# Optimization experiments

Measured on AMD Instinct MI355X. Metric: run time of the kernel, lower is better.

Reference implementation:

```python
import jax, jax.numpy as jnp
import numpy as np
from jax.experimental import sparse as jsparse

N_ITEMS = 20000   # item catalog size (S is [N_ITEMS, N_ITEMS])
N_USERS = 2048    # user batch
NNZ = 4_000_000


def setup_inputs() -> dict:
    key = jax.random.key(0)
    k1, k2, k3, k4 = jax.random.split(key, 4)
    X = jax.random.normal(k1, (N_USERS, N_ITEMS), dtype=jnp.float32)
    S_vals = jax.random.normal(k2, (NNZ,), dtype=jnp.float32)
    S_rows = jax.random.randint(k3, (NNZ,), 0, N_ITEMS, dtype=jnp.int32)
    S_cols = jax.random.randint(k4, (NNZ,), 0, N_ITEMS, dtype=jnp.int32)
    return {"X": X, "S_vals": S_vals, "S_rows": S_rows, "S_cols": S_cols}


def reference(X, S_vals, S_rows, S_cols):
    # torch.sparse.mm(S, X.t()).t()  ==  X @ S^T, with S sparse COO.
    indices = jnp.stack([S_rows, S_cols], axis=1)  # [nnz, 2]
    S = jsparse.BCOO((S_vals, indices), shape=(N_ITEMS, N_ITEMS))
    # (S @ X^T)^T -> [n_users, n_items]; duplicate indices sum, matching COO semantics.
    return (S @ X.T).T
```

## Files before the change

### kernel.cpp

```cpp
#include <hip/hip_runtime.h>

#define N_ITEMS 20000
#define N_USERS 2048
#define NNZ     4000000
#define LDP     2112
#define HALF_ITEMS 10000
#define CAP     320

typedef float    f32x4 __attribute__((ext_vector_type(4)));
typedef int      i32x4 __attribute__((ext_vector_type(4)));
typedef unsigned u32x4 __attribute__((ext_vector_type(4)));

#define OFF_XT     ((size_t)0)
#define OFF_CSRPK  ((size_t)84480000)
#define OFF_CNT    (OFF_CSRPK + 25600000)

static __device__ __forceinline__ unsigned short f2bf(float f) {
  unsigned u = __float_as_uint(f);
  unsigned r = (u + 0x7fffu + ((u >> 16) & 1u)) >> 16;
  return (unsigned short)r;
}

#define NSQ ((NNZ / 4 + 255) / 256)
#define NT_BLOCKS (313 * 32)

static __device__ __forceinline__ void scatter_body(
    const int* __restrict__ rows, const int* __restrict__ cols,
    const float* __restrict__ vals, int* __restrict__ cnt,
    unsigned* __restrict__ csr_pk, int pass, int b) {
  int i = (b * 256 + (int)threadIdx.x) * 4;
  if (i < NNZ) {
    i32x4 r4 = __builtin_nontemporal_load(reinterpret_cast<const i32x4*>(rows + i));
    i32x4 c4 = __builtin_nontemporal_load(reinterpret_cast<const i32x4*>(cols + i));
    f32x4 v4 = __builtin_nontemporal_load(reinterpret_cast<const f32x4*>(vals + i));
    #pragma unroll
    for (int k = 0; k < 4; ++k) {
      int r = r4[k];
      if ((unsigned)(r - pass * HALF_ITEMS) < (unsigned)HALF_ITEMS) {
        int pos = atomicAdd(&cnt[r], 1);
        if (pos >= CAP) pos = CAP - 1;
        csr_pk[r * CAP + pos] = ((unsigned)c4[k] << 16) | (unsigned)f2bf(v4[k]);
      }
    }
  }
}

__global__ __launch_bounds__(256) void scatterA_kernel(
    const int* __restrict__ rows, const int* __restrict__ cols,
    const float* __restrict__ vals, int* __restrict__ cnt,
    unsigned* __restrict__ csr_pk) {
  scatter_body(rows, cols, vals, cnt, csr_pk, 0, blockIdx.x);
}

__global__ __launch_bounds__(256) void prepB_kernel(
    const float* __restrict__ X, const int* __restrict__ rows,
    const int* __restrict__ cols, const float* __restrict__ vals,
    unsigned short* __restrict__ XT, int* __restrict__ cnt,
    unsigned* __restrict__ csr_pk) {
  int b = blockIdx.x;
  if (b < NSQ) {
    scatter_body(rows, cols, vals, cnt, csr_pk, 1, b);
  } else {
    __shared__ float tile[64][65];
    int b2 = b - NSQ;
    int k0 = (b2 % 313) * 64;
    int u0 = (b2 / 313) * 64;
    int lane = threadIdx.x & 63;
    int dq = threadIdx.x >> 6;
    #pragma unroll
    for (int m = 0; m < 16; ++m) {
      int u = u0 + dq + 4 * m;
      int k = k0 + lane;
      float v = 0.f;
      if (k < N_ITEMS)
        v = __builtin_nontemporal_load(&X[(size_t)u * N_ITEMS + k]);
      tile[lane][dq + 4 * m] = v;
    }
    __syncthreads();
    #pragma unroll
    for (int m = 0; m < 16; ++m) {
      int k = k0 + dq + 4 * m;
      if (k < N_ITEMS) {
        unsigned short s = f2bf(tile[dq + 4 * m][lane]);
        __builtin_nontemporal_store(s, &XT[(size_t)k * LDP + u0 + lane]);
      }
    }
  }
}

__global__ __launch_bounds__(256) void spmm_kernel(
    const int* __restrict__ cnt, const unsigned* __restrict__ csr_pk,
    const unsigned short* __restrict__ xt, float* __restrict__ out) {
  __shared__ float tile[16][132];
  int wg = blockIdx.x;
  int xcd = wg & 7;
  int slot = wg >> 3;
  int combo = slot / 1250;
  int rb = slot - combo * 1250;
  int uchunk = xcd * 2 + combo;
  int u0 = uchunk * 128;
  int r0 = rb * 16;
  int lane = threadIdx.x & 63;
  int wave = __builtin_amdgcn_readfirstlane((int)(threadIdx.x >> 6));
  const char* xtb = (const char*)(xt + u0);
  unsigned lane4 = 4 * (unsigned)lane;

#define LOAD8(E, BASE)                                                   \
  { u32x4 q0 = *reinterpret_cast<const u32x4*>(csr_pk + (BASE));         \
    u32x4 q1 = *reinterpret_cast<const u32x4*>(csr_pk + (BASE) + 4);     \
    E[0] = q0.x; E[1] = q0.y; E[2] = q0.z; E[3] = q0.w;                  \
    E[4] = q1.x; E[5] = q1.y; E[6] = q1.z; E[7] = q1.w; }
#define GATHER8(G, E)                                                    \
  { _Pragma("unroll")                                                    \
    for (int k = 0; k < 8; ++k)                                          \
      G[k] = *reinterpret_cast<const unsigned*>(                         \
          xtb + ((E[k] >> 16) * (unsigned)(LDP * 2) + lane4)); }
#define FMA8(G, E)                                                       \
  { _Pragma("unroll")                                                    \
    for (int k = 0; k < 8; ++k) {                                        \
      float v  = __uint_as_float(E[k] << 16);            \
      float xl = __uint_as_float(G[k] << 16);                            \
      float xh = __uint_as_float(G[k]);             \
      if (k & 1) { a2 = fmaf(v, xl, a2); a3 = fmaf(v, xh, a3); }         \
      else       { a0 = fmaf(v, xl, a0); a1 = fmaf(v, xh, a1); }         \
    } }

  #pragma unroll 1
  for (int rr = 0; rr < 4; ++rr) {
    int r = r0 + wave * 4 + rr;
    int jb = r * CAP;
    int cr = __builtin_amdgcn_readfirstlane(cnt[r]);
    if (cr > CAP) cr = CAP;
    int nb = (cr + 7) >> 3;
    float a0 = 0.f, a1 = 0.f, a2 = 0.f, a3 = 0.f;
    if (nb >= 3) {
      unsigned e0[8], e1[8], e2[8], g0[8], g1[8], g2[8];
      LOAD8(e0, jb)
      GATHER8(g0, e0)
      LOAD8(e1, jb + 8)
      GATHER8(g1, e1)
      LOAD8(e2, jb + 16)
      int b = 0;
      for (; b + 5 < nb; b += 3) {
        GATHER8(g2, e2)
        FMA8(g0, e0)
        LOAD8(e0, jb + (b + 3) * 8)
        GATHER8(g0, e0)
        FMA8(g1, e1)
        LOAD8(e1, jb + (b + 4) * 8)
        GATHER8(g1, e1)
        FMA8(g2, e2)
        LOAD8(e2, jb + (b + 5) * 8)
      }
      int m = nb - b;
      GATHER8(g2, e2)
      FMA8(g0, e0)
      if (m == 3) {
        FMA8(g1, e1)
        FMA8(g2, e2)
      } else if (m == 4) {
        LOAD8(e0, jb + (b + 3) * 8)
        GATHER8(g0, e0)
        FMA8(g1, e1)
        FMA8(g2, e2)
        FMA8(g0, e0)
      } else {
        LOAD8(e0, jb + (b + 3) * 8)
        GATHER8(g0, e0)
        FMA8(g1, e1)
        LOAD8(e1, jb + (b + 4) * 8)
        GATHER8(g1, e1)
        FMA8(g2, e2)
        FMA8(g0, e0)
        FMA8(g1, e1)
      }
    } else if (nb == 2) {
      unsigned e0[8], e1[8], g0[8], g1[8];
      LOAD8(e0, jb)
      GATHER8(g0, e0)
      LOAD8(e1, jb + 8)
      GATHER8(g1, e1)
      FMA8(g0, e0)
      FMA8(g1, e1)
    } else if (nb == 1) {
      unsigned e0[8], g0[8];
      LOAD8(e0, jb)
      GATHER8(g0, e0)
      FMA8(g0, e0)
    }
    tile[wave * 4 + rr][2 * lane]     = a0 + a2;
    tile[wave * 4 + rr][2 * lane + 1] = a1 + a3;
  }
#undef LOAD8
#undef GATHER8
#undef FMA8

  __syncthreads();
  int ul = threadIdx.x >> 1;
  int rseg = (threadIdx.x & 1) * 8;
  float* op = &out[(size_t)(u0 + ul) * N_ITEMS + r0 + rseg];
  f32x4 o0, o1;
  o0.x = tile[rseg + 0][ul]; o0.y = tile[rseg + 1][ul];
  o0.z = tile[rseg + 2][ul]; o0.w = tile[rseg + 3][ul];
  o1.x = tile[rseg + 4][ul]; o1.y = tile[rseg + 5][ul];
  o1.z = tile[rseg + 6][ul]; o1.w = tile[rseg + 7][ul];
  __builtin_nontemporal_store(o0, reinterpret_cast<f32x4*>(op));
  __builtin_nontemporal_store(o1, reinterpret_cast<f32x4*>(op) + 1);
}

extern "C" void kernel_launch(void* const* d_in, const int* in_sizes, int n_in,
                              void* d_out, int out_size, void* d_ws, size_t ws_size,
                              hipStream_t stream) {
  const float* X      = (const float*)d_in[0];
  const float* S_vals = (const float*)d_in[1];
  const int*   S_rows = (const int*)d_in[2];
  const int*   S_cols = (const int*)d_in[3];
  float* out = (float*)d_out;

  char* ws = (char*)d_ws;
  unsigned short* XT = (unsigned short*)(ws + OFF_XT);
  unsigned* csr_pk   = (unsigned*)(ws + OFF_CSRPK);
  int* cnt           = (int*)(ws + OFF_CNT);

  hipMemsetAsync(cnt, 0, N_ITEMS * sizeof(int), stream);
  hipMemsetAsync(csr_pk, 0, (size_t)N_ITEMS * CAP * sizeof(unsigned), stream);
  scatterA_kernel<<<NSQ, 256, 0, stream>>>(S_rows, S_cols, S_vals, cnt, csr_pk);
  prepB_kernel<<<NSQ + NT_BLOCKS, 256, 0, stream>>>(
      X, S_rows, S_cols, S_vals, XT, cnt, csr_pk);
  spmm_kernel<<<1250 * 16, 256, 0, stream>>>(cnt, csr_pk, XT, out);
}
```

Before: 1.071 ms.

## Drop CSR memset via exact-count tail loop and split transpose across prep kernels

The full 25.6MB memset of the padded CSR buffer is removed. The SpMM kernel now processes only whole 8-entry blocks and handles the remainder with a scalar tail loop, so it never reads uninitialized padding. The X transpose is also split in half between the two scatter kernels so each launch mixes atomic scatter work with bandwidth-bound transpose work. The cost is a serial tail loop per row (up to 7 dependent gathers) in place of the padded vector block.

```diff
diff --git a/kernel.cpp b/kernel.cpp
--- a/kernel.cpp
+++ b/kernel.cpp
@@ -22,7 +22,7 @@
 }
 
 #define NSQ ((NNZ / 4 + 255) / 256)
-#define NT_BLOCKS (313 * 32)
+#define NTH (313 * 16)
 
 static __device__ __forceinline__ void scatter_body(
     const int* __restrict__ rows, const int* __restrict__ cols,
@@ -45,11 +45,42 @@
   }
 }
 
-__global__ __launch_bounds__(256) void scatterA_kernel(
-    const int* __restrict__ rows, const int* __restrict__ cols,
-    const float* __restrict__ vals, int* __restrict__ cnt,
+static __device__ __forceinline__ void transpose_tile(
+    const float* __restrict__ X, unsigned short* __restrict__ XT,
+    int b2, int uoff) {
+  __shared__ float tile[64][65];
+  int k0 = (b2 % 313) * 64;
+  int u0 = (b2 / 313 + uoff) * 64;
+  int lane = threadIdx.x & 63;
+  int dq = threadIdx.x >> 6;
+  #pragma unroll
+  for (int m = 0; m < 16; ++m) {
+    int u = u0 + dq + 4 * m;
+    int k = k0 + lane;
+    float v = 0.f;
+    if (k < N_ITEMS)
+      v = __builtin_nontemporal_load(&X[(size_t)u * N_ITEMS + k]);
+    tile[lane][dq + 4 * m] = v;
+  }
+  __syncthreads();
+  #pragma unroll
+  for (int m = 0; m < 16; ++m) {
+    int k = k0 + dq + 4 * m;
+    if (k < N_ITEMS) {
+      unsigned short s = f2bf(tile[dq + 4 * m][lane]);
+      __builtin_nontemporal_store(s, &XT[(size_t)k * LDP + u0 + lane]);
+    }
+  }
+}
+
+__global__ __launch_bounds__(256) void prepA_kernel(
+    const float* __restrict__ X, const int* __restrict__ rows,
+    const int* __restrict__ cols, const float* __restrict__ vals,
+    unsigned short* __restrict__ XT, int* __restrict__ cnt,
     unsigned* __restrict__ csr_pk) {
-  scatter_body(rows, cols, vals, cnt, csr_pk, 0, blockIdx.x);
+  int b = blockIdx.x;
+  if (b < NSQ) scatter_body(rows, cols, vals, cnt, csr_pk, 0, b);
+  else         transpose_tile(X, XT, b - NSQ, 0);
 }
 
 __global__ __launch_bounds__(256) void prepB_kernel(
@@ -58,34 +89,8 @@
     unsigned short* __restrict__ XT, int* __restrict__ cnt,
     unsigned* __restrict__ csr_pk) {
   int b = blockIdx.x;
-  if (b < NSQ) {
-    scatter_body(rows, cols, vals, cnt, csr_pk, 1, b);
-  } else {
-    __shared__ float tile[64][65];
-    int b2 = b - NSQ;
-    int k0 = (b2 % 313) * 64;
-    int u0 = (b2 / 313) * 64;
-    int lane = threadIdx.x & 63;
-    int dq = threadIdx.x >> 6;
-    #pragma unroll
-    for (int m = 0; m < 16; ++m) {
-      int u = u0 + dq + 4 * m;
-      int k = k0 + lane;
-      float v = 0.f;
-      if (k < N_ITEMS)
-        v = __builtin_nontemporal_load(&X[(size_t)u * N_ITEMS + k]);
-      tile[lane][dq + 4 * m] = v;
-    }
-    __syncthreads();
-    #pragma unroll
-    for (int m = 0; m < 16; ++m) {
-      int k = k0 + dq + 4 * m;
-      if (k < N_ITEMS) {
-        unsigned short s = f2bf(tile[dq + 4 * m][lane]);
-        __builtin_nontemporal_store(s, &XT[(size_t)k * LDP + u0 + lane]);
-      }
-    }
-  }
+  if (b < NSQ) scatter_body(rows, cols, vals, cnt, csr_pk, 1, b);
+  else         transpose_tile(X, XT, b - NSQ, 16);
 }
 
 __global__ __launch_bounds__(256) void spmm_kernel(
@@ -131,7 +136,7 @@
     int jb = r * CAP;
     int cr = __builtin_amdgcn_readfirstlane(cnt[r]);
     if (cr > CAP) cr = CAP;
-    int nb = (cr + 7) >> 3;
+    int nb = cr >> 3;
     float a0 = 0.f, a1 = 0.f, a2 = 0.f, a3 = 0.f;
     if (nb >= 3) {
       unsigned e0[8], e1[8], e2[8], g0[8], g1[8], g2[8];
@@ -188,6 +193,14 @@
       GATHER8(g0, e0)
       FMA8(g0, e0)
     }
+    for (int j = jb + nb * 8; j < jb + cr; ++j) {
+      unsigned ee = csr_pk[j];
+      unsigned g = *reinterpret_cast<const unsigned*>(
+          xtb + ((ee >> 16) * (unsigned)(LDP * 2) + lane4));
+      float v = __uint_as_float(ee << 16);
+      a0 = fmaf(v, __uint_as_float(g << 16), a0);
+      a1 = fmaf(v, __uint_as_float(g), a1);
+    }
     tile[wave * 4 + rr][2 * lane]     = a0 + a2;
     tile[wave * 4 + rr][2 * lane + 1] = a1 + a3;
   }
@@ -223,9 +236,9 @@
   int* cnt           = (int*)(ws + OFF_CNT);
 
   hipMemsetAsync(cnt, 0, N_ITEMS * sizeof(int), stream);
-  hipMemsetAsync(csr_pk, 0, (size_t)N_ITEMS * CAP * sizeof(unsigned), stream);
-  scatterA_kernel<<<NSQ, 256, 0, stream>>>(S_rows, S_cols, S_vals, cnt, csr_pk);
-  prepB_kernel<<<NSQ + NT_BLOCKS, 256, 0, stream>>>(
+  prepA_kernel<<<NSQ + NTH, 256, 0, stream>>>(
+      X, S_rows, S_cols, S_vals, XT, cnt, csr_pk);
+  prepB_kernel<<<NSQ + NTH, 256, 0, stream>>>(
       X, S_rows, S_cols, S_vals, XT, cnt, csr_pk);
   spmm_kernel<<<1250 * 16, 256, 0, stream>>>(cnt, csr_pk, XT, out);
 }
```

Result: no change. 1.060 ms (-1.0%).
